# Kernel optimization log

Measured on AMD Instinct MI355X. Metric: run time of the kernel, lower is better.

## Reference

```python
import jax, jax.numpy as jnp
import numpy as np

N_WIRES = 8
N_LAYERS = 6
OUTPUT_DIM = 8
BATCH = 131072


def _rx(t):
    c = jnp.cos(t / 2).astype(jnp.complex64)
    s = jnp.sin(t / 2).astype(jnp.complex64)
    return jnp.stack([jnp.stack([c, -1j * s], -1), jnp.stack([-1j * s, c], -1)], -2)


def _ry(t):
    c = jnp.cos(t / 2).astype(jnp.complex64)
    s = jnp.sin(t / 2).astype(jnp.complex64)
    return jnp.stack([jnp.stack([c, -s], -1), jnp.stack([s, c], -1)], -2)


def _rz(t):
    e = jnp.exp(-0.5j * t.astype(jnp.complex64))
    z = jnp.zeros_like(e)
    return jnp.stack([jnp.stack([e, z], -1), jnp.stack([z, jnp.conj(e)], -1)], -2)


def _apply_1q(state, U, w):
    # state: [B, 2, 2, ..., 2]; U: [2,2] (shared) or [B,2,2] (per-batch angle)
    s = jnp.moveaxis(state, w + 1, -1)
    if U.ndim == 3:
        s = jnp.einsum('bij,b...j->b...i', U, s)
    else:
        s = jnp.einsum('ij,...j->...i', U, s)
    return jnp.moveaxis(s, -1, w + 1)


def _apply_cnot(state, c, t):
    s = jnp.moveaxis(state, (c + 1, t + 1), (-2, -1))
    s = jnp.concatenate([s[..., :1, :], s[..., 1:, ::-1]], axis=-2)
    return jnp.moveaxis(s, (-2, -1), (c + 1, t + 1))


def _circuit(x, weights):
    B = x.shape[0]
    dim = 2 ** N_WIRES
    state = jnp.zeros((B, dim), dtype=jnp.complex64).at[:, 0].set(1.0)
    state = state.reshape((B,) + (2,) * N_WIRES)
    rx0 = _rx(x[:, 0])  # [B,2,2] data-encoding gates (batched angles)
    ry1 = _ry(x[:, 1])
    for layer in range(N_LAYERS):
        for i in range(N_WIRES):
            state = _apply_1q(state, rx0 if i % 2 == 0 else ry1, i)
        for i in range(N_WIRES):
            state = _apply_1q(state, _rx(weights[layer, i, 0]), i)
            state = _apply_1q(state, _ry(weights[layer, i, 1]), i)
            state = _apply_1q(state, _rz(weights[layer, i, 2]), i)
        for i in range(N_WIRES - 1):
            state = _apply_cnot(state, i, i + 1)
    probs = state.real ** 2 + state.imag ** 2  # [B, 2,...,2]
    evs = []
    for i in range(OUTPUT_DIM):
        p = jnp.moveaxis(probs, i + 1, 1).reshape(B, 2, -1)
        evs.append((p[:, 0] - p[:, 1]).sum(-1))  # <Z_i>
    return jnp.stack(evs, 0)  # [output_dim, B]


def setup_inputs() -> dict:
    key = jax.random.key(0)
    k1, k2 = jax.random.split(key)
    x = jax.random.normal(k1, (BATCH, 2), dtype=jnp.float32)
    weights = jax.random.normal(k2, (N_LAYERS, N_WIRES, 3), dtype=jnp.float32)
    return {'x': x, 'weights': weights}


def reference(x, weights):
    basis_t = _circuit(x, weights) * jnp.pi  # [output_dim, B]
    return basis_t.T  # [B, output_dim]
```

## Files before the change

kernel.cpp:

```cpp
#include <hip/hip_runtime.h>
#include <math.h>

#define N_WIRES 8
#define N_LAYERS 6
#define NG 49
#define NG2 (NG * NG)

#define WS_E_OFF 0
#define WS_FB_OFF 76832

typedef _Float16 half8 __attribute__((ext_vector_type(8)));
typedef float f32x4 __attribute__((ext_vector_type(4)));

__global__ __launch_bounds__(256) void qnn_grid_lds(const float* __restrict__ w,
                                                    float* __restrict__ E) {
    __shared__ float gates[N_LAYERS * N_WIRES * 8];
    __shared__ float2 bufA[256];
    __shared__ float2 bufB[256];
    __shared__ float partial[4][8];

    const int tid = threadIdx.x;
    const int g = blockIdx.x;
    const int ga = (g * 1338) >> 16;
    const int gb = g - ga * NG;
    const float step = (float)(2.0 * M_PI / 49.0);

    if (tid < N_LAYERS * N_WIRES) {
        const int i = tid & 7;
        float wx = w[tid * 3 + 0], wy = w[tid * 3 + 1], wz = w[tid * 3 + 2];
        float sx, cx, sy, cy, sz, cz;
        sincosf(0.5f * wx, &sx, &cx);
        sincosf(0.5f * wy, &sy, &cy);
        sincosf(0.5f * wz, &sz, &cz);
        float A00r = cy * cx, A00i = sy * sx;
        float A01r = -sy * cx, A01i = -cy * sx;
        float A10r = sy * cx, A10i = -cy * sx;
        float A11r = cy * cx, A11i = -sy * sx;
        float U00r = A00r * cz + A00i * sz, U00i = A00i * cz - A00r * sz;
        float U01r = A01r * cz + A01i * sz, U01i = A01i * cz - A01r * sz;
        float U10r = A10r * cz - A10i * sz, U10i = A10i * cz + A10r * sz;
        float U11r = A11r * cz - A11i * sz, U11i = A11i * cz + A11r * sz;
        float V00r, V00i, V01r, V01i, V10r, V10i, V11r, V11i;
        if ((i & 1) == 0) {
            V00r = U01i; V00i = -U01r;
            V01r = U00i; V01i = -U00r;
            V10r = U11i; V10i = -U11r;
            V11r = U10i; V11i = -U10r;
        } else {
            V00r = U01r;  V00i = U01i;
            V01r = -U00r; V01i = -U00i;
            V10r = U11r;  V10i = U11i;
            V11r = -U10r; V11i = -U10i;
        }
        const float xx = (i & 1) ? (step * (float)gb) : (step * (float)ga);
        float se, ce;
        sincosf(0.5f * xx, &se, &ce);
        float* o = gates + tid * 8;
        o[0] = ce * U00r + se * V00r;  o[1] = ce * U00i + se * V00i;
        o[2] = ce * U01r + se * V01r;  o[3] = ce * U01i + se * V01i;
        o[4] = ce * U10r + se * V10r;  o[5] = ce * U10i + se * V10i;
        o[6] = ce * U11r + se * V11r;  o[7] = ce * U11i + se * V11i;
    }

    float ar = (tid == 0) ? 1.0f : 0.0f;
    float ai = 0.0f;
    __syncthreads();

    int flip = 0;
    for (int l = 0; l < N_LAYERS; ++l) {
        #pragma unroll
        for (int i = 0; i < 2; ++i) {
            const float* gm = gates + (l * 8 + i) * 8;
            const int p = 7 - i;
            const int m = 1 << p;
            const int bit = (tid >> p) & 1;
            float2* buf = flip ? bufB : bufA;
            flip ^= 1;
            buf[tid] = make_float2(ar, ai);
            __syncthreads();
            float2 other = buf[tid ^ m];
            float a0r = bit ? other.x : ar, a0i = bit ? other.y : ai;
            float a1r = bit ? ar : other.x, a1i = bit ? ai : other.y;
            float c0r = gm[bit * 4 + 0], c0i = gm[bit * 4 + 1];
            float c1r = gm[bit * 4 + 2], c1i = gm[bit * 4 + 3];
            float nr = c0r * a0r - c0i * a0i + c1r * a1r - c1i * a1i;
            float ni = c0r * a0i + c0i * a0r + c1r * a1i + c1i * a1r;
            ar = nr; ai = ni;
        }
        #pragma unroll
        for (int i = 2; i < 8; ++i) {
            const float* gm = gates + (l * 8 + i) * 8;
            const int p = 7 - i;
            const int m = 1 << p;
            const int bit = (tid >> p) & 1;
            float otr = __shfl_xor(ar, m);
            float oti = __shfl_xor(ai, m);
            float a0r = bit ? otr : ar, a0i = bit ? oti : ai;
            float a1r = bit ? ar : otr, a1i = bit ? ai : oti;
            float c0r = gm[bit * 4 + 0], c0i = gm[bit * 4 + 1];
            float c1r = gm[bit * 4 + 2], c1i = gm[bit * 4 + 3];
            float nr = c0r * a0r - c0i * a0i + c1r * a1r - c1i * a1i;
            float ni = c0r * a0i + c0i * a0r + c1r * a1i + c1i * a1r;
            ar = nr; ai = ni;
        }
        {
            float2* buf = flip ? bufB : bufA;
            flip ^= 1;
            buf[tid] = make_float2(ar, ai);
            __syncthreads();
            float2 src = buf[tid ^ (tid >> 1)];
            ar = src.x; ai = src.y;
        }
    }

    float p = ar * ar + ai * ai;
    float ev[8];
    #pragma unroll
    for (int i = 0; i < 8; ++i) ev[i] = ((tid >> (7 - i)) & 1) ? -p : p;
    #pragma unroll
    for (int i = 0; i < 8; ++i) {
        #pragma unroll
        for (int s = 1; s < 64; s <<= 1) ev[i] += __shfl_xor(ev[i], s);
    }
    const int wave = tid >> 6, lane = tid & 63;
    if (lane == 0) {
        #pragma unroll
        for (int i = 0; i < 8; ++i) partial[wave][i] = ev[i];
    }
    __syncthreads();
    if (tid < 8) {
        E[tid * NG2 + g] = partial[0][tid] + partial[1][tid] + partial[2][tid] + partial[3][tid];
    }
}

__global__ __launch_bounds__(64) void dft2(const float* __restrict__ E,
                                           _Float16* __restrict__ Fb) {
    const int kp = blockIdx.x, i = blockIdx.y, t = threadIdx.x;
    __shared__ float Es[NG2];
    __shared__ float H[NG];
    __shared__ float tc[NG], ts[NG];
    const float step = (float)(2.0 * M_PI / 49.0);
    const float PI = 3.14159265358979323846f;

    if (t < NG) {
        float s, c;
        sincosf(step * (float)t, &s, &c);
        tc[t] = c; ts[t] = s;
    }
    if (kp < NG) {
        for (int e = t; e < NG2; e += 64) Es[e] = E[i * NG2 + e];
    }
    __syncthreads();

    if (kp < NG && t < NG) {
        const int b = t;
        const int n = (kp + 1) >> 1;
        const bool use_cos = (kp & 1) || (kp == 0);
        float acc = 0.f;
        int j = 0;
        for (int a = 0; a < NG; ++a) {
            acc = fmaf(Es[a * NG + b], use_cos ? tc[j] : ts[j], acc);
            j += n; if (j >= NG) j -= NG;
        }
        acc *= (kp == 0) ? (1.0f / 49.0f) : (2.0f / 49.0f);
        H[b] = acc;
    }
    __syncthreads();

    const int l = t;
    float acc = 0.f;
    if (kp < NG && l < NG) {
        const int n = (l + 1) >> 1;
        const bool use_cos = (l & 1) || (l == 0);
        int j = 0;
        for (int b = 0; b < NG; ++b) {
            acc = fmaf(H[b], use_cos ? tc[j] : ts[j], acc);
            j += n; if (j >= NG) j -= NG;
        }
        acc *= (l == 0) ? (PI / 49.0f) : (2.0f * PI / 49.0f);
    }
    {
        const int ntile = kp >> 4, n = kp & 15;
        const int chunk = l >> 5, lrem = l & 31;
        const int q = lrem >> 3, j = lrem & 7;
        const int fid = (i * 4 + ntile) * 2 + chunk;
        Fb[fid * 512 + (q * 16 + n) * 8 + j] = (_Float16)acc;
    }
}

#define V0PAD 68

__global__ __launch_bounds__(256) void contract_mfma(const float* __restrict__ x,
                                                     const _Float16* __restrict__ Fb,
                                                     float* __restrict__ out, int B) {
    __shared__ float xs0[64], xs1[64];
    __shared__ float v0t[64 * V0PAD];

    const int tid = threadIdx.x;
    const int bbase = blockIdx.x * 64;
    if (bbase >= B) return;

    if (tid < 64) {
        float2 xv = ((const float2*)x)[bbase + tid];
        xs0[tid] = xv.x;
        xs1[tid] = xv.y;
    }
    __syncthreads();

    {
        const int b = tid & 63, s = tid >> 6;
        const float x0 = xs0[b];
        float c1, s1;
        sincosf(x0, &s1, &c1);
        float cb, sb;
        sincosf((float)(8 * s) * x0, &sb, &cb);
        float* row = v0t + b * V0PAD + 16 * s;
        const int k0 = 16 * s;
        row[0] = (k0 == 0) ? 1.0f : ((k0 < NG) ? sb : 0.0f);
        float cm = cb, sm = sb;
        #pragma unroll
        for (int j = 1; j < 16; ++j) {
            if (j & 1) {
                float c2 = cm * c1 - sm * s1, s2 = sm * c1 + cm * s1;
                cm = c2; sm = s2;
            }
            float val = (j & 1) ? cm : sm;
            row[j] = ((k0 + j) < NG) ? val : 0.0f;
        }
    }

    const int lane = tid & 63;
    const int w = tid >> 6;
    const int q = lane >> 4;

    const float x1v = xs1[w * 16 + (lane & 15)];
    float c1, s1;
    sincosf(x1v, &s1, &c1);
    half8 afrag[2];
    #pragma unroll
    for (int c = 0; c < 2; ++c) {
        const int l0 = c * 32 + q * 8;
        float cb, sb;
        sincosf((float)(l0 >> 1) * x1v, &sb, &cb);
        float vals[8];
        vals[0] = (l0 == 0) ? 1.0f : sb;
        float cm = cb, sm = sb;
        #pragma unroll
        for (int j = 1; j < 8; ++j) {
            if (j & 1) {
                float c2 = cm * c1 - sm * s1, s2 = sm * c1 + cm * s1;
                cm = c2; sm = s2;
            }
            vals[j] = (j & 1) ? cm : sm;
        }
        #pragma unroll
        for (int j = 0; j < 8; ++j) {
            afrag[c][j] = (_Float16)(((l0 + j) < 52) ? vals[j] : 0.0f);
        }
    }

    __syncthreads();

    const half8* FB = (const half8*)Fb;

    #pragma unroll 1
    for (int ip = 0; ip < 4; ++ip) {
        const int i0 = ip * 2;

        half8 bfrag[16];
        #pragma unroll
        for (int ii = 0; ii < 2; ++ii)
            #pragma unroll
            for (int nt = 0; nt < 4; ++nt)
                #pragma unroll
                for (int c = 0; c < 2; ++c) {
                    const int fid = ((i0 + ii) * 4 + nt) * 2 + c;
                    bfrag[(ii * 4 + nt) * 2 + c] = FB[fid * 64 + lane];
                }

        f32x4 acc[8];
        #pragma unroll
        for (int t = 0; t < 8; ++t) {
            f32x4 z = {0.f, 0.f, 0.f, 0.f};
            acc[t] = __builtin_amdgcn_mfma_f32_16x16x32_f16(afrag[0], bfrag[t * 2 + 0], z, 0, 0, 0);
            acc[t] = __builtin_amdgcn_mfma_f32_16x16x32_f16(afrag[1], bfrag[t * 2 + 1], acc[t], 0, 0, 0);
        }

        float res[2][4];
        #pragma unroll
        for (int ii = 0; ii < 2; ++ii)
            #pragma unroll
            for (int r = 0; r < 4; ++r) res[ii][r] = 0.f;

        #pragma unroll
        for (int ii = 0; ii < 2; ++ii)
            #pragma unroll
            for (int nt = 0; nt < 4; ++nt) {
                f32x4 a = acc[ii * 4 + nt];
                #pragma unroll
                for (int r = 0; r < 4; ++r) {
                    const int bloc = w * 16 + q * 4 + r;
                    float v0 = v0t[bloc * V0PAD + nt * 16 + (lane & 15)];
                    res[ii][r] = fmaf(a[r], v0, res[ii][r]);
                }
            }

        #pragma unroll
        for (int ii = 0; ii < 2; ++ii)
            #pragma unroll
            for (int r = 0; r < 4; ++r) {
                float v = res[ii][r];
                v += __shfl_xor(v, 1);
                v += __shfl_xor(v, 2);
                v += __shfl_xor(v, 4);
                v += __shfl_xor(v, 8);
                res[ii][r] = v;
            }

        if ((lane & 15) == 0) {
            #pragma unroll
            for (int r = 0; r < 4; ++r) {
                const int b = bbase + w * 16 + q * 4 + r;
                out[(size_t)b * 8 + i0 + 0] = res[0][r];
                out[(size_t)b * 8 + i0 + 1] = res[1][r];
            }
        }
    }
}

extern "C" void kernel_launch(void* const* d_in, const int* in_sizes, int n_in,
                              void* d_out, int out_size, void* d_ws, size_t ws_size,
                              hipStream_t stream) {
    (void)n_in; (void)out_size; (void)ws_size;
    const float* x = (const float*)d_in[0];
    const float* w = (const float*)d_in[1];
    float* out = (float*)d_out;
    char* ws = (char*)d_ws;
    float* E = (float*)(ws + WS_E_OFF);
    _Float16* Fb = (_Float16*)(ws + WS_FB_OFF);
    const int B = in_sizes[0] / 2;

    hipLaunchKernelGGL(qnn_grid_lds, dim3(NG2), dim3(256), 0, stream, w, E);
    hipLaunchKernelGGL(dft2, dim3(64, 8), dim3(64), 0, stream, E, Fb);
    hipLaunchKernelGGL(contract_mfma, dim3((B + 63) / 64, 1), dim3(256), 0, stream,
                       x, Fb, out, B);
}
```

Measured before the change: 107.0 us.

## Swap warp work split so each warp keeps its B fragments and loops over batch groups

Each warp now owns one output pair (two wires) and loads its 16 B fragments from global once, issuing the loads before the trig setup so their latency overlaps it. The A fragments for all four batch groups are staged in LDS, and each warp loops over batch groups instead of output pairs. Previously every warp re-read all B fragments four times per block. The change adds LDS traffic for the A fragments and writes each output pair as a single float2 store.

```diff
diff --git a/kernel.cpp b/kernel.cpp
--- a/kernel.cpp
+++ b/kernel.cpp
@@ -195,10 +195,20 @@
                                                      float* __restrict__ out, int B) {
     __shared__ float xs0[64], xs1[64];
     __shared__ float v0t[64 * V0PAD];
+    __shared__ __align__(16) half8 aS[2 * 4 * 64];
 
     const int tid = threadIdx.x;
     const int bbase = blockIdx.x * 64;
     if (bbase >= B) return;
+
+    const int lane = tid & 63;
+    const int w = tid >> 6;
+    const int q = lane >> 4;
+
+    const half8* FB = (const half8*)Fb;
+    half8 bfrag[16];
+    #pragma unroll
+    for (int f = 0; f < 16; ++f) bfrag[f] = FB[(w * 16 + f) * 64 + lane];
 
     if (tid < 64) {
         float2 xv = ((const float2*)x)[bbase + tid];
@@ -229,61 +239,48 @@
         }
     }
 
-    const int lane = tid & 63;
-    const int w = tid >> 6;
-    const int q = lane >> 4;
-
-    const float x1v = xs1[w * 16 + (lane & 15)];
-    float c1, s1;
-    sincosf(x1v, &s1, &c1);
-    half8 afrag[2];
-    #pragma unroll
-    for (int c = 0; c < 2; ++c) {
-        const int l0 = c * 32 + q * 8;
-        float cb, sb;
-        sincosf((float)(l0 >> 1) * x1v, &sb, &cb);
-        float vals[8];
-        vals[0] = (l0 == 0) ? 1.0f : sb;
-        float cm = cb, sm = sb;
-        #pragma unroll
-        for (int j = 1; j < 8; ++j) {
-            if (j & 1) {
-                float c2 = cm * c1 - sm * s1, s2 = sm * c1 + cm * s1;
-                cm = c2; sm = s2;
-            }
-            vals[j] = (j & 1) ? cm : sm;
-        }
-        #pragma unroll
-        for (int j = 0; j < 8; ++j) {
-            afrag[c][j] = (_Float16)(((l0 + j) < 52) ? vals[j] : 0.0f);
-        }
-    }
-
-    __syncthreads();
-
-    const half8* FB = (const half8*)Fb;
+    {
+        const float x1v = xs1[w * 16 + (lane & 15)];
+        float c1, s1;
+        sincosf(x1v, &s1, &c1);
+        #pragma unroll
+        for (int c = 0; c < 2; ++c) {
+            const int l0 = c * 32 + q * 8;
+            float cb, sb;
+            sincosf((float)(l0 >> 1) * x1v, &sb, &cb);
+            float vals[8];
+            vals[0] = (l0 == 0) ? 1.0f : sb;
+            float cm = cb, sm = sb;
+            #pragma unroll
+            for (int j = 1; j < 8; ++j) {
+                if (j & 1) {
+                    float c2 = cm * c1 - sm * s1, s2 = sm * c1 + cm * s1;
+                    cm = c2; sm = s2;
+                }
+                vals[j] = (j & 1) ? cm : sm;
+            }
+            half8 af;
+            #pragma unroll
+            for (int j = 0; j < 8; ++j) {
+                af[j] = (_Float16)(((l0 + j) < 52) ? vals[j] : 0.0f);
+            }
+            aS[(c * 4 + w) * 64 + lane] = af;
+        }
+    }
+
+    __syncthreads();
 
     #pragma unroll 1
-    for (int ip = 0; ip < 4; ++ip) {
-        const int i0 = ip * 2;
-
-        half8 bfrag[16];
-        #pragma unroll
-        for (int ii = 0; ii < 2; ++ii)
-            #pragma unroll
-            for (int nt = 0; nt < 4; ++nt)
-                #pragma unroll
-                for (int c = 0; c < 2; ++c) {
-                    const int fid = ((i0 + ii) * 4 + nt) * 2 + c;
-                    bfrag[(ii * 4 + nt) * 2 + c] = FB[fid * 64 + lane];
-                }
+    for (int bg = 0; bg < 4; ++bg) {
+        const half8 a0 = aS[(0 * 4 + bg) * 64 + lane];
+        const half8 a1 = aS[(1 * 4 + bg) * 64 + lane];
 
         f32x4 acc[8];
         #pragma unroll
         for (int t = 0; t < 8; ++t) {
             f32x4 z = {0.f, 0.f, 0.f, 0.f};
-            acc[t] = __builtin_amdgcn_mfma_f32_16x16x32_f16(afrag[0], bfrag[t * 2 + 0], z, 0, 0, 0);
-            acc[t] = __builtin_amdgcn_mfma_f32_16x16x32_f16(afrag[1], bfrag[t * 2 + 1], acc[t], 0, 0, 0);
+            acc[t] = __builtin_amdgcn_mfma_f32_16x16x32_f16(a0, bfrag[t * 2 + 0], z, 0, 0, 0);
+            acc[t] = __builtin_amdgcn_mfma_f32_16x16x32_f16(a1, bfrag[t * 2 + 1], acc[t], 0, 0, 0);
         }
 
         float res[2][4];
@@ -299,7 +296,7 @@
                 f32x4 a = acc[ii * 4 + nt];
                 #pragma unroll
                 for (int r = 0; r < 4; ++r) {
-                    const int bloc = w * 16 + q * 4 + r;
+                    const int bloc = bg * 16 + q * 4 + r;
                     float v0 = v0t[bloc * V0PAD + nt * 16 + (lane & 15)];
                     res[ii][r] = fmaf(a[r], v0, res[ii][r]);
                 }
@@ -320,9 +317,9 @@
         if ((lane & 15) == 0) {
             #pragma unroll
             for (int r = 0; r < 4; ++r) {
-                const int b = bbase + w * 16 + q * 4 + r;
-                out[(size_t)b * 8 + i0 + 0] = res[0][r];
-                out[(size_t)b * 8 + i0 + 1] = res[1][r];
+                const int b = bbase + bg * 16 + q * 4 + r;
+                float2 st = make_float2(res[0][r], res[1][r]);
+                *(float2*)&out[(size_t)b * 8 + 2 * w] = st;
             }
         }
     }
```

Result: faster. 103.8 us (-3.0%).
